# Optimization experiments

Measured on AMD Instinct MI355X. Metric: run time of the kernel, lower is better.

## Reference

```python
import jax, jax.numpy as jnp
import numpy as np

N_NODE = 100000
N_EDGE = 500000
IN_DIM = 128
OUT_DIM = 128
ATTN_DIM = 64
N_REL = 200
N_Q = 64


def setup_inputs() -> dict:
    key = jax.random.key(0)
    ks = jax.random.split(key, 24)
    # edge table: columns [r_idx, _, rel, _, tau, sub, obj]
    r_idx = jax.random.randint(ks[0], (N_EDGE,), 0, N_Q, dtype=jnp.int32)
    rel = jax.random.randint(ks[1], (N_EDGE,), 0, 2 * N_REL + 1, dtype=jnp.int32)
    tau = jax.random.randint(ks[2], (N_EDGE,), -1, 366, dtype=jnp.int32)  # -1 -> q_tau fallback
    sub = jax.random.randint(ks[3], (N_EDGE,), 0, N_NODE, dtype=jnp.int32)
    obj = jax.random.randint(ks[4], (N_EDGE,), 0, N_NODE, dtype=jnp.int32)
    zeros = jnp.zeros((N_EDGE,), jnp.int32)
    edges = jnp.stack([r_idx, zeros, rel, zeros, tau, sub, obj], axis=1)

    def lin(k, fan_in, fan_out):
        return jax.random.normal(k, (fan_in, fan_out), jnp.float32) * (1.0 / np.sqrt(fan_in))

    return {
        "q_sub": jax.random.randint(ks[5], (N_Q,), 0, N_NODE, dtype=jnp.int32),
        "q_rel": jax.random.randint(ks[6], (N_Q,), 0, 2 * N_REL + 1, dtype=jnp.int32),
        "q_tau": 180,
        "hidden": jax.random.normal(ks[7], (N_NODE, IN_DIM), jnp.float32),
        "edges": edges,
        "n_node": N_NODE,
        "old_nodes_new_idx": jax.random.randint(ks[8], (1000,), 0, N_NODE, dtype=jnp.int32),
        "rela_embed": jax.random.normal(ks[9], (2 * N_REL + 1, IN_DIM), jnp.float32),
        "Ws_w": lin(ks[10], IN_DIM, ATTN_DIM),
        "Wr_w": lin(ks[11], IN_DIM, ATTN_DIM),
        "Wqr_w": lin(ks[12], IN_DIM, ATTN_DIM),
        "Wqr_b": jnp.zeros((ATTN_DIM,), jnp.float32),
        "Wtau_w": lin(ks[13], IN_DIM, ATTN_DIM),
        "w_alpha_w": lin(ks[14], ATTN_DIM, 1),
        "w_alpha_b": jnp.zeros((1,), jnp.float32),
        "W_h_w": lin(ks[15], IN_DIM, OUT_DIM),
        "W_h_s_w": lin(ks[16], IN_DIM, OUT_DIM),
        "weight_t1": jax.random.normal(ks[17], (1, IN_DIM), jnp.float32),
        "bias_t1": jax.random.normal(ks[18], (1, IN_DIM), jnp.float32),
        "weight_t2": jax.random.normal(ks[19], (1, IN_DIM), jnp.float32),
        "bias_t2": jax.random.normal(ks[20], (1, IN_DIM), jnp.float32),
    }


def reference(q_sub, q_rel, q_tau, hidden, edges, n_node, old_nodes_new_idx,
              rela_embed, Ws_w, Wr_w, Wqr_w, Wqr_b, Wtau_w,
              w_alpha_w, w_alpha_b, W_h_w, W_h_s_w,
              weight_t1, bias_t1, weight_t2, bias_t2):
    sub = edges[:, 5]
    rel = edges[:, 2]
    obj = edges[:, 6]
    tau = edges[:, 4]
    r_idx = edges[:, 0]

    hs = hidden[sub]                       # [E, in_dim] gather
    hr = rela_embed[rel]                   # [E, in_dim]
    h_qr = rela_embed[q_rel][r_idx]        # [E, in_dim]

    tau = jnp.where(tau >= 0, tau, q_tau)
    delta = (tau - q_tau).astype(hidden.dtype)[:, None]  # [E, 1]
    h_tau = weight_t1 * delta + bias_t1 + jnp.sin(weight_t2 * delta + bias_t2)

    message = hs + hr + h_tau              # [E, in_dim]

    attn = jax.nn.relu(hs @ Ws_w + hr @ Wr_w + (h_qr @ Wqr_w + Wqr_b) + h_tau @ Wtau_w)
    alpha = jax.nn.sigmoid(attn @ w_alpha_w + w_alpha_b)  # [E, 1]

    msg = alpha * message
    msg_s = (1.0 - alpha) * message

    agg = jax.ops.segment_sum(msg, obj, num_segments=n_node)      # [n_node, in_dim]
    agg_s = jax.ops.segment_sum(msg_s, obj, num_segments=n_node)

    hidden_new = agg @ W_h_w       # act is identity (default lambda x: x)
    hidden_new_s = agg_s @ W_h_s_w
    return hidden_new, hidden_new_s
```

## Files before the change

kernel.cpp:

```cpp
#include <hip/hip_runtime.h>
#include <math.h>

#define N_NODE   100000
#define N_EDGE   500000
#define IN_DIM   128
#define OUT_DIM  128
#define ATTN_DIM 64
#define N_RELTAB 401
#define N_QRY    64
#define N_TAU    366

#define SCAN_BLK     256
#define N_SCAN_BLKS  ((N_NODE + SCAN_BLK - 1) / SCAN_BLK)

#define NB_TABLES    (N_TAU + N_RELTAB + N_QRY + 3)
#define NB_COUNT     ((N_EDGE + 255) / 256)
#define NB_NODE      ((N_NODE + 63) / 64)

typedef unsigned int  uint;
typedef unsigned short ushort;
typedef __attribute__((ext_vector_type(8))) short bf16x8;
typedef __attribute__((ext_vector_type(4))) float f32x4;

__device__ __forceinline__ float bfl(uint u)  { return __uint_as_float(u << 16); }
__device__ __forceinline__ float bfh(uint u)  { return __uint_as_float(u & 0xFFFF0000u); }
__device__ __forceinline__ uint  f2bfbits(float f) {
    uint u = __float_as_uint(f);
    return (u + 0x7FFFu + ((u >> 16) & 1u)) >> 16;
}
__device__ __forceinline__ uint  pack2(float lo, float hi) {
    return f2bfbits(lo) | (f2bfbits(hi) << 16);
}

__global__ __launch_bounds__(256) void build_count(const int* __restrict__ q_rel,
                             const int* __restrict__ q_tau_p,
                             const float* __restrict__ rela_embed,
                             const float* __restrict__ Wr_w,
                             const float* __restrict__ Wqr_w,
                             const float* __restrict__ Wqr_b,
                             const float* __restrict__ Wtau_w,
                             const float* __restrict__ w_t1,
                             const float* __restrict__ b_t1,
                             const float* __restrict__ w_t2,
                             const float* __restrict__ b_t2,
                             const float* __restrict__ W_h_w,
                             const float* __restrict__ W_h_s_w,
                             const float* __restrict__ Ws_w,
                             const int* __restrict__ edges,
                             uint* __restrict__ rel_attn_bf,
                             uint* __restrict__ qr_attn_bf,
                             uint* __restrict__ tau_attn_bf,
                             uint* __restrict__ rel_msg_bf,
                             uint* __restrict__ tau_msg_bf,
                             ushort* __restrict__ wfrag_bf,
                             ushort* __restrict__ wsT_bf,
                             int* __restrict__ count) {
    __shared__ float srow[IN_DIM];
    __shared__ float sattn[ATTN_DIM];
    const int b = blockIdx.x;
    const int t = threadIdx.x;

    if (b >= NB_TABLES) {
        const int e = (b - NB_TABLES) * 256 + t;
        if (e < N_EDGE) {
            const int obj = edges[(size_t)e * 7 + 6];
            atomicAdd(&count[obj], 1);
        }
        return;
    }

    if (b < N_TAU) {
        if (t < 128) {
            const int q_tau = *q_tau_p;
            const float delta = (float)(b - q_tau);
            srow[t] = w_t1[t] * delta + b_t1[t] + sinf(w_t2[t] * delta + b_t2[t]);
        }
        __syncthreads();
        if (t < 64) tau_msg_bf[b * 64 + t] = pack2(srow[2 * t], srow[2 * t + 1]);
        if (t < ATTN_DIM) {
            float acc = 0.f;
            #pragma unroll 8
            for (int d = 0; d < IN_DIM; ++d)
                acc += srow[d] * Wtau_w[d * ATTN_DIM + t];
            sattn[t] = acc;
        }
        __syncthreads();
        if (t < 32) tau_attn_bf[b * 32 + t] = pack2(sattn[2 * t], sattn[2 * t + 1]);
    } else if (b < N_TAU + N_RELTAB) {
        const int r = b - N_TAU;
        if (t < 128) srow[t] = rela_embed[r * IN_DIM + t];
        __syncthreads();
        if (t < 64) rel_msg_bf[r * 64 + t] = pack2(srow[2 * t], srow[2 * t + 1]);
        if (t < ATTN_DIM) {
            float acc = 0.f;
            #pragma unroll 8
            for (int d = 0; d < IN_DIM; ++d)
                acc += srow[d] * Wr_w[d * ATTN_DIM + t];
            sattn[t] = acc;
        }
        __syncthreads();
        if (t < 32) rel_attn_bf[r * 32 + t] = pack2(sattn[2 * t], sattn[2 * t + 1]);
    } else if (b < N_TAU + N_RELTAB + N_QRY) {
        const int i = b - N_TAU - N_RELTAB;
        const int r = q_rel[i];
        if (t < 128) srow[t] = rela_embed[r * IN_DIM + t];
        __syncthreads();
        if (t < ATTN_DIM) {
            float acc = Wqr_b[t];
            #pragma unroll 8
            for (int d = 0; d < IN_DIM; ++d)
                acc += srow[d] * Wqr_w[d * ATTN_DIM + t];
            sattn[t] = acc;
        }
        __syncthreads();
        if (t < 32) qr_attn_bf[i * 32 + t] = pack2(sattn[2 * t], sattn[2 * t + 1]);
    } else {
        const int w = b - (N_TAU + N_RELTAB + N_QRY);
        if (w < 2) {
            const float* Wsrc = w ? W_h_s_w : W_h_w;
            ushort* dst = wfrag_bf + (size_t)w * 2048 * 8;
            for (int r = 0; r < 8; ++r) {
                const int s  = t * 8 + r;
                const int ct = s >> 8;
                const int ks = (s >> 6) & 3;
                const int l  = s & 63;
                const int lm = l & 15;
                const int lq = l >> 4;
                union { ushort us[8]; uint4 v; } tmp;
                #pragma unroll
                for (int j = 0; j < 8; ++j)
                    tmp.us[j] = (ushort)f2bfbits(Wsrc[(ks * 32 + lq * 8 + j) * 128 + ct * 16 + lm]);
                *(uint4*)(dst + (size_t)s * 8) = tmp.v;
            }
        } else {
            if (t < 128)
                for (int n = 0; n < 64; ++n)
                    wsT_bf[n * 128 + t] = (ushort)f2bfbits(Ws_w[t * ATTN_DIM + n]);
        }
    }
}

__global__ __launch_bounds__(256) void node_attn_scan(const float* __restrict__ hidden,
                                                      const ushort* __restrict__ wsT_bf,
                                                      uint* __restrict__ hid_bf_u,
                                                      ushort* __restrict__ A_node,
                                                      const int* __restrict__ count,
                                                      int* __restrict__ partial) {
    __shared__ int slds[SCAN_BLK];

    if (blockIdx.x >= NB_NODE) {
        const int blk = blockIdx.x - NB_NODE;
        const int i = blk * SCAN_BLK + threadIdx.x;
        slds[threadIdx.x] = (i < N_NODE) ? count[i] : 0;
        __syncthreads();
        for (int s = SCAN_BLK / 2; s > 0; s >>= 1) {
            if (threadIdx.x < s) slds[threadIdx.x] += slds[threadIdx.x + s];
            __syncthreads();
        }
        if (threadIdx.x == 0) partial[blk] = slds[0];
        return;
    }

    const int wave = threadIdx.x >> 6;
    const int lane = threadIdx.x & 63;
    const int m    = lane & 15;
    const int quad = lane >> 4;
    const int row0 = blockIdx.x * 64 + wave * 16;
    const int row  = row0 + m;
    const int rowc = min(row, N_NODE - 1);

    const float* hsrc = hidden + (size_t)rowc * IN_DIM;
    ushort* hdst = (ushort*)hid_bf_u + (size_t)rowc * 128;

    bf16x8 afr[4];
    #pragma unroll
    for (int ks = 0; ks < 4; ++ks) {
        const int k0 = ks * 32 + quad * 8;
        const float4 v0 = *(const float4*)(hsrc + k0);
        const float4 v1 = *(const float4*)(hsrc + k0 + 4);
        union { uint u[4]; bf16x8 v; } cvt;
        cvt.u[0] = pack2(v0.x, v0.y);
        cvt.u[1] = pack2(v0.z, v0.w);
        cvt.u[2] = pack2(v1.x, v1.y);
        cvt.u[3] = pack2(v1.z, v1.w);
        afr[ks] = cvt.v;
        if (row < N_NODE) *(bf16x8*)(hdst + k0) = cvt.v;
    }

    f32x4 acc[4] = {};
    #pragma unroll
    for (int ks = 0; ks < 4; ++ks) {
        #pragma unroll
        for (int ct = 0; ct < 4; ++ct) {
            const bf16x8 wfr = *(const bf16x8*)(wsT_bf + (ct * 16 + m) * 128 + ks * 32 + quad * 8);
            acc[ct] = __builtin_amdgcn_mfma_f32_16x16x32_bf16(wfr, afr[ks], acc[ct], 0, 0, 0);
        }
    }

    if (row < N_NODE) {
        #pragma unroll
        for (int ct = 0; ct < 4; ++ct) {
            uint2 pk;
            pk.x = pack2(acc[ct][0], acc[ct][1]);
            pk.y = pack2(acc[ct][2], acc[ct][3]);
            *(uint2*)(A_node + (size_t)row * 64 + ct * 16 + quad * 4) = pk;
        }
    }
}

__global__ __launch_bounds__(512) void scan_partials(const int* __restrict__ partial,
                                                     int* __restrict__ blk_off) {
    __shared__ int lds[512];
    const int t = threadIdx.x;
    lds[t] = (t < N_SCAN_BLKS) ? partial[t] : 0;
    __syncthreads();
    for (int d = 1; d < 512; d <<= 1) {
        int v = (t >= d) ? lds[t - d] : 0;
        __syncthreads();
        lds[t] += v;
        __syncthreads();
    }
    if (t < N_SCAN_BLKS) blk_off[t] = (t == 0) ? 0 : lds[t - 1];
}

__global__ __launch_bounds__(SCAN_BLK) void scan_apply(const int* __restrict__ count,
                                                       const int* __restrict__ blk_off,
                                                       int* __restrict__ off,
                                                       int* __restrict__ cursor) {
    __shared__ int lds[SCAN_BLK];
    const int t = threadIdx.x;
    const int i = blockIdx.x * SCAN_BLK + t;
    const int v = (i < N_NODE) ? count[i] : 0;
    lds[t] = v;
    __syncthreads();
    for (int d = 1; d < SCAN_BLK; d <<= 1) {
        int x = (t >= d) ? lds[t - d] : 0;
        __syncthreads();
        lds[t] += x;
        __syncthreads();
    }
    const int excl = blk_off[blockIdx.x] + lds[t] - v;
    if (i < N_NODE) { off[i] = excl; cursor[i] = excl; }
    if (i == N_NODE - 1) off[N_NODE] = excl + v;
}

__global__ __launch_bounds__(256) void alpha_fill(const int* __restrict__ edges,
                                                  const int* __restrict__ q_tau_p,
                                                  const uint* __restrict__ A_node_bf,
                                                  const uint* __restrict__ rel_attn_bf,
                                                  const uint* __restrict__ qr_attn_bf,
                                                  const uint* __restrict__ tau_attn_bf,
                                                  const float* __restrict__ w_alpha_w,
                                                  const float* __restrict__ w_alpha_b,
                                                  int* __restrict__ cursor,
                                                  int4* __restrict__ recs) {
    const int t = threadIdx.x;
    const int q = t & 3;
    const int e = blockIdx.x * 64 + (t >> 2);
    if (e >= N_EDGE) return;

    const int* ed = edges + (size_t)e * 7;
    const int r_idx = ed[0];
    const int rel   = ed[2];
    const int tau   = ed[4];
    const int sub   = ed[5];
    const int obj   = ed[6];
    const int q_tau = *q_tau_p;
    const int tidx  = (tau >= 0) ? tau : q_tau;

    const uint4*  pa = (const uint4*)(A_node_bf  + (size_t)sub * 32) + q * 2;
    const uint4*  pr = (const uint4*)(rel_attn_bf + rel   * 32) + q * 2;
    const uint4*  pq = (const uint4*)(qr_attn_bf  + r_idx * 32) + q * 2;
    const uint4*  pt = (const uint4*)(tau_attn_bf + tidx  * 32) + q * 2;
    const float4* wv = (const float4*)w_alpha_w + q * 4;

    float acc = 0.f;

#define DOT_UINT(va, vr, vq, vt, wlo, whi) do {                                  \
        const float x0 = bfl(va) + bfl(vr) + bfl(vq) + bfl(vt);                  \
        const float x1 = bfh(va) + bfh(vr) + bfh(vq) + bfh(vt);                  \
        acc = fmaf(fmaxf(x0, 0.f), (wlo), fmaf(fmaxf(x1, 0.f), (whi), acc));     \
    } while (0)

    #pragma unroll
    for (int c = 0; c < 2; ++c) {
        const uint4  ua = pa[c];
        const uint4  ur = pr[c];
        const uint4  uq = pq[c];
        const uint4  ut = pt[c];
        const float4 w0 = wv[c * 2];
        const float4 w1 = wv[c * 2 + 1];
        DOT_UINT(ua.x, ur.x, uq.x, ut.x, w0.x, w0.y);
        DOT_UINT(ua.y, ur.y, uq.y, ut.y, w0.z, w0.w);
        DOT_UINT(ua.z, ur.z, uq.z, ut.z, w1.x, w1.y);
        DOT_UINT(ua.w, ur.w, uq.w, ut.w, w1.z, w1.w);
    }
#undef DOT_UINT

    acc += __shfl_xor(acc, 1, 64);
    acc += __shfl_xor(acc, 2, 64);

    if (q == 0) {
        const float alpha = 1.f / (1.f + __expf(-(acc + w_alpha_b[0])));
        const int pos = atomicAdd(&cursor[obj], 1);
        recs[pos] = make_int4(sub, rel, tidx, __float_as_int(alpha));
    }
}

__global__ __launch_bounds__(256) void agg_gemm(const int* __restrict__ off,
                                                const int4* __restrict__ recs,
                                                const uint* __restrict__ hid_bf,
                                                const uint* __restrict__ rel_msg_bf,
                                                const uint* __restrict__ tau_msg_bf,
                                                const ushort* __restrict__ wfrag,
                                                float* __restrict__ out) {
    __shared__ uint lagg[2 * 16 * 64];

    const int wave = threadIdx.x >> 6;
    const int lane = threadIdx.x & 63;
    const int tile = blockIdx.x * 16;

    #pragma unroll
    for (int k = 0; k < 4; ++k) {
        const int n16 = wave * 4 + k;
        const int n = tile + n16;
        const int j0 = off[n];
        const int j1 = off[n + 1];

        float t0 = 0.f, t1 = 0.f;
        float a0 = 0.f, a1 = 0.f;
        int j = j0;
        for (; j + 1 < j1; j += 2) {
            const int4 rA = recs[j];
            const int4 rB = recs[j + 1];
            const uint hA = hid_bf[(size_t)rA.x * 64 + lane];
            const uint hB = hid_bf[(size_t)rB.x * 64 + lane];
            const uint eA = rel_msg_bf[rA.y * 64 + lane];
            const uint eB = rel_msg_bf[rB.y * 64 + lane];
            const uint uA = tau_msg_bf[rA.z * 64 + lane];
            const uint uB = tau_msg_bf[rB.z * 64 + lane];
            const float alA = __int_as_float(rA.w);
            const float alB = __int_as_float(rB.w);
            const float m0A = bfl(hA) + bfl(eA) + bfl(uA);
            const float m1A = bfh(hA) + bfh(eA) + bfh(uA);
            const float m0B = bfl(hB) + bfl(eB) + bfl(uB);
            const float m1B = bfh(hB) + bfh(eB) + bfh(uB);
            t0 += m0A + m0B;  t1 += m1A + m1B;
            a0 = fmaf(alA, m0A, fmaf(alB, m0B, a0));
            a1 = fmaf(alA, m1A, fmaf(alB, m1B, a1));
        }
        if (j < j1) {
            const int4 rA = recs[j];
            const uint hA = hid_bf[(size_t)rA.x * 64 + lane];
            const uint eA = rel_msg_bf[rA.y * 64 + lane];
            const uint uA = tau_msg_bf[rA.z * 64 + lane];
            const float alA = __int_as_float(rA.w);
            const float m0A = bfl(hA) + bfl(eA) + bfl(uA);
            const float m1A = bfh(hA) + bfh(eA) + bfh(uA);
            t0 += m0A;  t1 += m1A;
            a0 = fmaf(alA, m0A, a0);
            a1 = fmaf(alA, m1A, a1);
        }
        const int gw = (((lane >> 2) ^ (n16 & 7)) << 2) | (lane & 3);
        lagg[n16 * 64 + gw]        = pack2(a0, a1);
        lagg[1024 + n16 * 64 + gw] = pack2(t0 - a0, t1 - a1);
    }
    __syncthreads();

    const int half = wave & 1;
    const int ctg  = (wave >> 1) * 4;
    const int m    = lane & 15;
    const int quad = lane >> 4;

    bf16x8 bfrag[4];
    #pragma unroll
    for (int ks = 0; ks < 4; ++ks) {
        const int g = (ks * 4 + quad) ^ (m & 7);
        bfrag[ks] = *(const bf16x8*)&lagg[half * 1024 + m * 64 + g * 4];
    }

    f32x4 acc[4] = {};
    #pragma unroll
    for (int ks = 0; ks < 4; ++ks) {
        #pragma unroll
        for (int c = 0; c < 4; ++c) {
            const bf16x8 wfr = *(const bf16x8*)(wfrag +
                ((size_t)(((half * 8 + ctg + c) * 4 + ks) * 64 + lane)) * 8);
            acc[c] = __builtin_amdgcn_mfma_f32_16x16x32_bf16(wfr, bfrag[ks], acc[c], 0, 0, 0);
        }
    }

    float* O = out + (size_t)half * N_NODE * 128 + (size_t)(tile + m) * 128;
    #pragma unroll
    for (int c = 0; c < 4; ++c)
        *(f32x4*)(O + (ctg + c) * 16 + quad * 4) = acc[c];
}

extern "C" void kernel_launch(void* const* d_in, const int* in_sizes, int n_in,
                              void* d_out, int out_size, void* d_ws, size_t ws_size,
                              hipStream_t stream) {
    const int*   q_rel      = (const int*)d_in[1];
    const int*   q_tau_p    = (const int*)d_in[2];
    const float* hidden     = (const float*)d_in[3];
    const int*   edges      = (const int*)d_in[4];
    const float* rela_embed = (const float*)d_in[7];
    const float* Ws_w       = (const float*)d_in[8];
    const float* Wr_w       = (const float*)d_in[9];
    const float* Wqr_w      = (const float*)d_in[10];
    const float* Wqr_b      = (const float*)d_in[11];
    const float* Wtau_w     = (const float*)d_in[12];
    const float* w_alpha_w  = (const float*)d_in[13];
    const float* w_alpha_b  = (const float*)d_in[14];
    const float* W_h_w      = (const float*)d_in[15];
    const float* W_h_s_w    = (const float*)d_in[16];
    const float* w_t1       = (const float*)d_in[17];
    const float* b_t1       = (const float*)d_in[18];
    const float* w_t2       = (const float*)d_in[19];
    const float* b_t2       = (const float*)d_in[20];

    char* p = (char*)d_ws;
    uint* hid_bf      = (uint*)p;                 p += (size_t)N_NODE * 64 * 4;
    uint* A_node_bf   = (uint*)p;                 p += (size_t)N_NODE * 32 * 4;
    int4* recs        = (int4*)p;                 p += (size_t)N_EDGE * 16;
    uint* rel_attn_bf = (uint*)p;                 p += N_RELTAB * 32 * 4;
    uint* qr_attn_bf  = (uint*)p;                 p += N_QRY * 32 * 4;
    uint* tau_attn_bf = (uint*)p;                 p += N_TAU * 32 * 4;
    uint* rel_msg_bf  = (uint*)p;                 p += N_RELTAB * 64 * 4;
    uint* tau_msg_bf  = (uint*)p;                 p += N_TAU * 64 * 4;
    ushort* wfrag_bf  = (ushort*)p;               p += (size_t)2 * 2048 * 8 * 2;
    ushort* wsT_bf    = (ushort*)p;               p += (size_t)64 * 128 * 2;
    int*  count       = (int*)p;                  p += N_NODE * 4;
    int*  off         = (int*)p;                  p += (N_NODE + 1) * 4;
    int*  cursor      = (int*)p;                  p += N_NODE * 4;
    int*  partial     = (int*)p;                  p += N_SCAN_BLKS * 4;
    int*  blk_off     = (int*)p;                  p += N_SCAN_BLKS * 4;

    hipMemsetAsync(count, 0, (size_t)N_NODE * sizeof(int), stream);

    build_count<<<dim3(NB_TABLES + NB_COUNT), dim3(256), 0, stream>>>(
        q_rel, q_tau_p, rela_embed, Wr_w, Wqr_w, Wqr_b, Wtau_w,
        w_t1, b_t1, w_t2, b_t2, W_h_w, W_h_s_w, Ws_w, edges,
        rel_attn_bf, qr_attn_bf, tau_attn_bf, rel_msg_bf, tau_msg_bf,
        wfrag_bf, wsT_bf, count);

    node_attn_scan<<<dim3(NB_NODE + N_SCAN_BLKS), dim3(256), 0, stream>>>(
        hidden, wsT_bf, hid_bf, (ushort*)A_node_bf, count, partial);

    scan_partials<<<dim3(1), dim3(512), 0, stream>>>(partial, blk_off);
    scan_apply<<<dim3(N_SCAN_BLKS), dim3(SCAN_BLK), 0, stream>>>(count, blk_off, off, cursor);

    alpha_fill<<<dim3((N_EDGE + 63) / 64), dim3(256), 0, stream>>>(
        edges, q_tau_p, A_node_bf, rel_attn_bf, qr_attn_bf, tau_attn_bf,
        w_alpha_w, w_alpha_b, cursor, recs);

    agg_gemm<<<dim3(N_NODE / 16), dim3(256), 0, stream>>>(
        off, recs, hid_bf, rel_msg_bf, tau_msg_bf, wfrag_bf, (float*)d_out);
}
```

Baseline: 322.8 us.

## Merge scan kernels, pre-scale record indices, stage edge records in LDS

Removes the single-block scan_partials launch: each scan_apply block now sums the preceding block partials itself with a tree reduction. alpha_fill stores row offsets pre-multiplied by 64 so agg_gemm skips the index multiplies. agg_gemm loads all edge records for its 16-node tile into shared memory with one cooperative coalesced load, falling back to global reads when a tile has more than 768 records. The cost is extra LDS use that may lower occupancy, plus redundant partial sums in every scan block.

```diff
diff --git a/kernel.cpp b/kernel.cpp
--- a/kernel.cpp
+++ b/kernel.cpp
@@ -16,6 +16,8 @@
 #define NB_TABLES    (N_TAU + N_RELTAB + N_QRY + 3)
 #define NB_COUNT     ((N_EDGE + 255) / 256)
 #define NB_NODE      ((N_NODE + 63) / 64)
+
+#define REC_CAP      768
 
 typedef unsigned int  uint;
 typedef unsigned short ushort;
@@ -208,28 +210,28 @@
     }
 }
 
-__global__ __launch_bounds__(512) void scan_partials(const int* __restrict__ partial,
-                                                     int* __restrict__ blk_off) {
-    __shared__ int lds[512];
-    const int t = threadIdx.x;
-    lds[t] = (t < N_SCAN_BLKS) ? partial[t] : 0;
-    __syncthreads();
-    for (int d = 1; d < 512; d <<= 1) {
-        int v = (t >= d) ? lds[t - d] : 0;
-        __syncthreads();
-        lds[t] += v;
-        __syncthreads();
-    }
-    if (t < N_SCAN_BLKS) blk_off[t] = (t == 0) ? 0 : lds[t - 1];
-}
-
 __global__ __launch_bounds__(SCAN_BLK) void scan_apply(const int* __restrict__ count,
-                                                       const int* __restrict__ blk_off,
+                                                       const int* __restrict__ partial,
                                                        int* __restrict__ off,
                                                        int* __restrict__ cursor) {
     __shared__ int lds[SCAN_BLK];
+    __shared__ int base_s;
     const int t = threadIdx.x;
-    const int i = blockIdx.x * SCAN_BLK + t;
+    const int b = blockIdx.x;
+
+    int s = 0;
+    if (t < b) s += partial[t];
+    if (t + 256 < b) s += partial[t + 256];
+    lds[t] = s;
+    __syncthreads();
+    for (int d = SCAN_BLK / 2; d > 0; d >>= 1) {
+        if (t < d) lds[t] += lds[t + d];
+        __syncthreads();
+    }
+    if (t == 0) base_s = lds[0];
+    __syncthreads();
+
+    const int i = b * SCAN_BLK + t;
     const int v = (i < N_NODE) ? count[i] : 0;
     lds[t] = v;
     __syncthreads();
@@ -239,7 +241,7 @@
         lds[t] += x;
         __syncthreads();
     }
-    const int excl = blk_off[blockIdx.x] + lds[t] - v;
+    const int excl = base_s + lds[t] - v;
     if (i < N_NODE) { off[i] = excl; cursor[i] = excl; }
     if (i == N_NODE - 1) off[N_NODE] = excl + v;
 }
@@ -303,7 +305,7 @@
     if (q == 0) {
         const float alpha = 1.f / (1.f + __expf(-(acc + w_alpha_b[0])));
         const int pos = atomicAdd(&cursor[obj], 1);
-        recs[pos] = make_int4(sub, rel, tidx, __float_as_int(alpha));
+        recs[pos] = make_int4(sub * 64, rel * 64, tidx * 64, __float_as_int(alpha));
     }
 }
 
@@ -315,56 +317,81 @@
                                                 const ushort* __restrict__ wfrag,
                                                 float* __restrict__ out) {
     __shared__ uint lagg[2 * 16 * 64];
+    __shared__ int4 lrec[REC_CAP];
 
     const int wave = threadIdx.x >> 6;
     const int lane = threadIdx.x & 63;
     const int tile = blockIdx.x * 16;
 
+    const int base = off[tile];
+    const int cnt  = off[tile + 16] - base;
+    const int ldn  = min(cnt, REC_CAP);
+    for (int i = threadIdx.x; i < ldn; i += 256)
+        lrec[i] = recs[base + i];
+    __syncthreads();
+
+#define ACC_EDGE2(rA, rB, haveB) do {                                            \
+        const uint hA = hid_bf[(uint)rA.x + lane];                               \
+        const uint eA = rel_msg_bf[rA.y + lane];                                 \
+        const uint uA = tau_msg_bf[rA.z + lane];                                 \
+        const float alA = __int_as_float(rA.w);                                  \
+        const float m0A = bfl(hA) + bfl(eA) + bfl(uA);                           \
+        const float m1A = bfh(hA) + bfh(eA) + bfh(uA);                           \
+        t0 += m0A;  t1 += m1A;                                                   \
+        a0 = fmaf(alA, m0A, a0);  a1 = fmaf(alA, m1A, a1);                       \
+        if (haveB) {                                                             \
+            const uint hB = hid_bf[(uint)rB.x + lane];                           \
+            const uint eB = rel_msg_bf[rB.y + lane];                             \
+            const uint uB = tau_msg_bf[rB.z + lane];                             \
+            const float alB = __int_as_float(rB.w);                              \
+            const float m0B = bfl(hB) + bfl(eB) + bfl(uB);                       \
+            const float m1B = bfh(hB) + bfh(eB) + bfh(uB);                       \
+            t0 += m0B;  t1 += m1B;                                               \
+            a0 = fmaf(alB, m0B, a0);  a1 = fmaf(alB, m1B, a1);                   \
+        }                                                                        \
+    } while (0)
+
     #pragma unroll
     for (int k = 0; k < 4; ++k) {
         const int n16 = wave * 4 + k;
         const int n = tile + n16;
-        const int j0 = off[n];
-        const int j1 = off[n + 1];
+        const int j0 = off[n] - base;
+        const int j1 = off[n + 1] - base;
 
         float t0 = 0.f, t1 = 0.f;
         float a0 = 0.f, a1 = 0.f;
-        int j = j0;
-        for (; j + 1 < j1; j += 2) {
-            const int4 rA = recs[j];
-            const int4 rB = recs[j + 1];
-            const uint hA = hid_bf[(size_t)rA.x * 64 + lane];
-            const uint hB = hid_bf[(size_t)rB.x * 64 + lane];
-            const uint eA = rel_msg_bf[rA.y * 64 + lane];
-            const uint eB = rel_msg_bf[rB.y * 64 + lane];
-            const uint uA = tau_msg_bf[rA.z * 64 + lane];
-            const uint uB = tau_msg_bf[rB.z * 64 + lane];
-            const float alA = __int_as_float(rA.w);
-            const float alB = __int_as_float(rB.w);
-            const float m0A = bfl(hA) + bfl(eA) + bfl(uA);
-            const float m1A = bfh(hA) + bfh(eA) + bfh(uA);
-            const float m0B = bfl(hB) + bfl(eB) + bfl(uB);
-            const float m1B = bfh(hB) + bfh(eB) + bfh(uB);
-            t0 += m0A + m0B;  t1 += m1A + m1B;
-            a0 = fmaf(alA, m0A, fmaf(alB, m0B, a0));
-            a1 = fmaf(alA, m1A, fmaf(alB, m1B, a1));
-        }
-        if (j < j1) {
-            const int4 rA = recs[j];
-            const uint hA = hid_bf[(size_t)rA.x * 64 + lane];
-            const uint eA = rel_msg_bf[rA.y * 64 + lane];
-            const uint uA = tau_msg_bf[rA.z * 64 + lane];
-            const float alA = __int_as_float(rA.w);
-            const float m0A = bfl(hA) + bfl(eA) + bfl(uA);
-            const float m1A = bfh(hA) + bfh(eA) + bfh(uA);
-            t0 += m0A;  t1 += m1A;
-            a0 = fmaf(alA, m0A, a0);
-            a1 = fmaf(alA, m1A, a1);
-        }
+
+        if (j1 <= REC_CAP) {
+            int j = j0;
+            for (; j + 1 < j1; j += 2) {
+                const int4 rA = lrec[j];
+                const int4 rB = lrec[j + 1];
+                ACC_EDGE2(rA, rB, true);
+            }
+            if (j < j1) {
+                const int4 rA = lrec[j];
+                const int4 rB = rA;
+                ACC_EDGE2(rA, rB, false);
+            }
+        } else {
+            int j = j0;
+            for (; j + 1 < j1; j += 2) {
+                const int4 rA = recs[base + j];
+                const int4 rB = recs[base + j + 1];
+                ACC_EDGE2(rA, rB, true);
+            }
+            if (j < j1) {
+                const int4 rA = recs[base + j];
+                const int4 rB = rA;
+                ACC_EDGE2(rA, rB, false);
+            }
+        }
+
         const int gw = (((lane >> 2) ^ (n16 & 7)) << 2) | (lane & 3);
         lagg[n16 * 64 + gw]        = pack2(a0, a1);
         lagg[1024 + n16 * 64 + gw] = pack2(t0 - a0, t1 - a1);
     }
+#undef ACC_EDGE2
     __syncthreads();
 
     const int half = wave & 1;
@@ -446,8 +473,7 @@
     node_attn_scan<<<dim3(NB_NODE + N_SCAN_BLKS), dim3(256), 0, stream>>>(
         hidden, wsT_bf, hid_bf, (ushort*)A_node_bf, count, partial);
 
-    scan_partials<<<dim3(1), dim3(512), 0, stream>>>(partial, blk_off);
-    scan_apply<<<dim3(N_SCAN_BLKS), dim3(SCAN_BLK), 0, stream>>>(count, blk_off, off, cursor);
+    scan_apply<<<dim3(N_SCAN_BLKS), dim3(SCAN_BLK), 0, stream>>>(count, partial, off, cursor);
 
     alpha_fill<<<dim3((N_EDGE + 63) / 64), dim3(256), 0, stream>>>(
         edges, q_tau_p, A_node_bf, rel_attn_bf, qr_attn_bf, tau_attn_bf,
```

Measured after the change: 310.7 us. 1.04x faster.
